# Optimization experiments

Hardware: AMD Instinct MI355X
Metric: run time of the kernel (lower is better)

## Reference

```python
import jax, jax.numpy as jnp
import numpy as np
from functools import partial

RED = 128      # reduced_dim
MK = 24        # r2d_m * r2d_k
HD, WD = 32, 16  # depth feature grid after 3 stride-2 convs on 256x128


def _conv(x, w, b):
    # torch Conv2d(k=3, stride=2, padding=1), NCHW / OIHW
    y = jax.lax.conv_general_dilated(
        x, w, window_strides=(2, 2), padding=((1, 1), (1, 1)),
        dimension_numbers=("NCHW", "OIHW", "NCHW"))
    return y + b[None, :, None, None]


def setup_inputs() -> dict:
    key = jax.random.key(0)
    ks = jax.random.split(key, 24)
    B = 64
    s = 0.02
    inp = {
        "features": jax.random.normal(ks[0], (B, 129, 768), jnp.float32),
        "d": jax.random.uniform(ks[1], (B, 1, 256, 128), jnp.float32),
        "W_rg": jax.random.normal(ks[2], (768, RED), jnp.float32) * s,
        "b_rg": jnp.zeros((RED,), jnp.float32),
        "W_rl": jax.random.normal(ks[3], (768, RED), jnp.float32) * s,
        "b_rl": jnp.zeros((RED,), jnp.float32),
        "conv1_w": jax.random.normal(ks[4], (64, 1, 3, 3), jnp.float32) * s,
        "conv1_b": jnp.zeros((64,), jnp.float32),
        "conv2_w": jax.random.normal(ks[5], (128, 64, 3, 3), jnp.float32) * s,
        "conv2_b": jnp.zeros((128,), jnp.float32),
        "conv3_w": jax.random.normal(ks[6], (128, 128, 3, 3), jnp.float32) * s,
        "conv3_b": jnp.zeros((128,), jnp.float32),
        "g_depth": jax.random.normal(ks[7], (RED,), jnp.float32),
        "W_merge": jax.random.normal(ks[8], (2 * RED, RED), jnp.float32) * s,
        "b_merge": jnp.zeros((RED,), jnp.float32),
        "W_q": jax.random.normal(ks[9], (2 * RED, RED), jnp.float32) * s,
        "b_q": jnp.zeros((RED,), jnp.float32),
        "W_v": jax.random.normal(ks[10], (RED, RED), jnp.float32) * s,
        "b_v": jnp.zeros((RED,), jnp.float32),
        "W_sel": jax.random.normal(ks[11], (RED, 3 * MK), jnp.float32) * s,
        "b_sel": jnp.zeros((3 * MK,), jnp.float32),
        "W_cls": jax.random.normal(ks[12], (RED, 751), jnp.float32) * s,
    }
    return inp


def _forward(features, d, W_rg, b_rg, W_rl, b_rl, conv1_w, conv1_b, conv2_w,
             conv2_b, conv3_w, conv3_b, g_depth, W_merge, b_merge, W_q, b_q,
             W_v, b_v, W_sel, b_sel, W_cls):
    B = features.shape[0]
    N = features.shape[1] - 1
    global_feat = features[:, 0] @ W_rg + b_rg                 # (B, 128)
    local_feat = features[:, 1:] @ W_rl + b_rl                 # (B, N, 128)
    lcg = jnp.concatenate(
        [jnp.broadcast_to(global_feat[:, None], (B, N, RED)), local_feat], -1)

    dep = _conv(_conv(_conv(d, conv1_w, conv1_b), conv2_w, conv2_b),
                conv3_w, conv3_b)                              # (B,128,32,16)
    dep = dep.transpose(0, 2, 3, 1).reshape(B, HD * WD, RED)
    lcgd = jnp.concatenate(
        [jnp.broadcast_to(g_depth[None, None], (B, HD * WD, RED)), dep], -1)
    lcgd = lcgd @ W_merge + b_merge

    q = lcg @ W_q + b_q                                        # (B,N,128)
    v = lcgd @ W_v + b_v                                       # (B,512,128)
    sel = jax.nn.sigmoid(q @ W_sel + b_sel)                    # (B,N,72)
    lx = sel[:, :, 0:2 * MK:2]                                 # (B,N,24)
    ly = sel[:, :, 1:2 * MK:2]
    attn = jax.nn.softmax(sel[:, :, 2 * MK:], axis=-1)

    # integer corner grid (original uses // stride == floor(loc*(dim-1)))
    x1 = jnp.floor(lx * (WD - 1))
    x2 = jnp.minimum(x1 + 1.0, float(WD - 1))
    y1 = jnp.floor(ly * (HD - 1))
    y2 = jnp.minimum(y1 + 1.0, float(HD - 1))
    xi1, xi2 = x1.astype(jnp.int32), x2.astype(jnp.int32)
    yi1, yi2 = y1.astype(jnp.int32), y2.astype(jnp.int32)

    # faithful to original gather: index = x_idx * Wd + y_idx
    gather = jax.vmap(lambda vb, ib: vb[ib])                   # (512,C),(N,K)->(N,K,C)
    f0 = gather(v, xi1 * WD + yi2)
    f1 = gather(v, xi2 * WD + yi2)
    f2 = gather(v, xi2 * WD + yi1)
    f3 = gather(v, xi1 * WD + yi1)

    # query coordinates scaled by full grid size (as in the original)
    x = lx * WD
    y = ly * HD
    w_ = x2 - x1
    h_ = y2 - y1
    degenerate = (h_ == 0) | (w_ == 0)
    denom = jnp.where(h_ * w_ == 0, 1.0, h_ * w_)
    coeff = jnp.where(degenerate, 2.0, 1.0 / denom)            # (B,N,24)
    xv0 = jnp.where(w_ == 0, 1.0, x2 - x)
    xv1 = jnp.where(w_ == 0, 1.0, x - x1)
    yv0 = jnp.where(h_ == 0, 1.0, y2 - y)
    yv1 = jnp.where(h_ == 0, 1.0, y - y1)

    # xv^T @ [[f0,f1],[f2,f3]] @ yv, per channel
    interp = coeff[..., None] * (
        xv0[..., None] * (f0 * yv0[..., None] + f1 * yv1[..., None]) +
        xv1[..., None] * (f2 * yv0[..., None] + f3 * yv1[..., None]))

    r2d_feat = jnp.mean(interp * attn[..., None], axis=-2)     # (B,N,128)
    final_embedding = jnp.mean(r2d_feat, axis=1)               # (B,128)
    cls_score = final_embedding @ W_cls                        # (B,751)
    return cls_score, final_embedding


def reference(features, d, W_rg, b_rg, W_rl, b_rl, conv1_w, conv1_b, conv2_w,
              conv2_b, conv3_w, conv3_b, g_depth, W_merge, b_merge, W_q, b_q,
              W_v, b_v, W_sel, b_sel, W_cls):
    return _forward(features, d, W_rg, b_rg, W_rl, b_rl, conv1_w, conv1_b,
                    conv2_w, conv2_b, conv3_w, conv3_b, g_depth, W_merge,
                    b_merge, W_q, b_q, W_v, b_v, W_sel, b_sel, W_cls)
```

## Files before the change

### kernel.cpp

```cpp
#include <hip/hip_runtime.h>
#include <hip/hip_bf16.h>


typedef __attribute__((ext_vector_type(8))) short short8;
typedef __attribute__((ext_vector_type(4))) short shortx4;
typedef __attribute__((ext_vector_type(4))) float floatx4;
typedef __attribute__((ext_vector_type(4))) int intx4;

#define MFMA16(a, b, c) __builtin_amdgcn_mfma_f32_16x16x32_bf16(a, b, c, 0, 0, 0)

__global__ __launch_bounds__(256) void prep_a(
    const float* __restrict__ W_q, const float* __restrict__ W_sel,
    const float* __restrict__ W_merge, const float* __restrict__ W_v,
    const float* __restrict__ g_depth, const float* __restrict__ b_merge,
    const float* __restrict__ features, const float* __restrict__ W_rg,
    const float* __restrict__ b_rg, const float* __restrict__ c2w,
    const float* __restrict__ c3w,
    float* __restrict__ W_qs, float* __restrict__ W_mv,
    float* __restrict__ c0, float* __restrict__ gfeat,
    __hip_bfloat16* __restrict__ w2t, __hip_bfloat16* __restrict__ w3t)
{
    __shared__ float fr_s[768];
    int bid = blockIdx.x, t = threadIdx.x;
    if (bid < 72) {
        int j = bid;
        float acc = 0.f;
        for (int k = 0; k < 128; ++k)
            acc = fmaf(W_q[t * 128 + k], W_sel[k * 72 + j], acc);
        W_qs[t * 72 + j] = acc;
    } else if (bid < 200) {
        int j = bid - 72;
        if (t < 128) {
            float acc = 0.f;
            for (int k = 0; k < 128; ++k)
                acc = fmaf(W_merge[(128 + t) * 128 + k], W_v[k * 128 + j], acc);
            W_mv[t * 128 + j] = acc;
        }
    } else if (bid == 200) {
        if (t < 128) {
            float acc = b_merge[t];
            for (int k = 0; k < 128; ++k)
                acc = fmaf(g_depth[k], W_merge[k * 128 + t], acc);
            c0[t] = acc;
        }
    } else if (bid < 265) {
        int row = bid - 201;
        for (int l = t; l < 768; l += 256)
            fr_s[l] = features[(long)row * 129 * 768 + l];
        __syncthreads();
        if (t < 128) {
            float acc = b_rg[t];
            for (int k = 0; k < 768; ++k)
                acc = fmaf(fr_s[k], W_rg[k * 128 + t], acc);
            gfeat[row * 128 + t] = acc;
        }
    } else if (bid < 553) {
        int idx = (bid - 265) * 256 + t;
        if (idx < 128 * 576) {
            int oc = idx / 576, k = idx % 576;
            int s = k >> 6, ic = k & 63;
            w2t[idx] = __float2bfloat16(c2w[oc * 576 + ic * 9 + s]);
        }
    } else {
        int idx = (bid - 553) * 256 + t;
        if (idx < 128 * 1152) {
            int oc = idx / 1152, k = idx % 1152;
            int s = k >> 7, ic = k & 127;
            w3t[idx] = __float2bfloat16(c3w[oc * 1152 + ic * 9 + s]);
        }
    }
}

__global__ __launch_bounds__(256) void prep2_k(
    const float* __restrict__ W_rl, const float* __restrict__ W_qs,
    const float* __restrict__ W_sel, const float* __restrict__ b_rl,
    const float* __restrict__ b_q, const float* __restrict__ b_sel,
    const float* __restrict__ gfeat, const float* __restrict__ c0,
    const float* __restrict__ W_v, const float* __restrict__ b_v,
    float* __restrict__ W_big, float* __restrict__ rowbias,
    float* __restrict__ c0v)
{
    int bid = blockIdx.x, t = threadIdx.x;
    if (bid < 216) {
        int j = bid / 3;
        int i = (bid % 3) * 256 + t;
        float acc = 0.f;
        for (int k = 0; k < 128; ++k)
            acc = fmaf(W_rl[i * 128 + k], W_qs[(128 + k) * 72 + j], acc);
        W_big[i * 72 + j] = acc;
    } else if (bid < 288) {
        int j = bid - 216;
        if (t < 64) {
            float vb = b_sel[j];
            for (int k = 0; k < 128; ++k) {
                vb = fmaf(b_rl[k], W_qs[(128 + k) * 72 + j], vb);
                vb = fmaf(b_q[k], W_sel[k * 72 + j], vb);
            }
            float acc = vb;
            for (int k = 0; k < 128; ++k)
                acc = fmaf(gfeat[t * 128 + k], W_qs[k * 72 + j], acc);
            rowbias[t * 72 + j] = acc;
        }
    } else {
        if (t < 128) {
            float acc = b_v[t];
            for (int k = 0; k < 128; ++k)
                acc = fmaf(c0[k], W_v[k * 128 + t], acc);
            c0v[t] = acc;
        }
    }
}

__global__ __launch_bounds__(256) void prep_b(
    const float* __restrict__ W_mv, const float* __restrict__ W_big,
    __hip_bfloat16* __restrict__ Bh, __hip_bfloat16* __restrict__ Bl,
    __hip_bfloat16* __restrict__ Wbh, __hip_bfloat16* __restrict__ Wbl)
{
    int bid = blockIdx.x, t = threadIdx.x;
    if (bid < 64) {
        int idx = bid * 256 + t;
        int n = idx >> 7, k = idx & 127;
        float w = W_mv[k * 128 + n];
        __hip_bfloat16 h = __float2bfloat16(w);
        Bh[idx] = h;
        Bl[idx] = __float2bfloat16(w - __bfloat162float(h));
    } else {
        int idx = (bid - 64) * 256 + t;
        if (idx < 80 * 768) {
            int n = idx / 768, k = idx - n * 768;
            float w = (n < 72) ? W_big[k * 72 + n] : 0.f;
            __hip_bfloat16 h = __float2bfloat16(w);
            Wbh[idx] = h;
            Wbl[idx] = __float2bfloat16(w - __bfloat162float(h));
        }
    }
}

__global__ __launch_bounds__(256) void conv1_k(
    const float* __restrict__ d, const float* __restrict__ w,
    const float* __restrict__ bias, __hip_bfloat16* __restrict__ out)
{
    __shared__ float in_s[9][130];
    __shared__ float ws_[576];
    __shared__ float bs_[64];
    int tid = threadIdx.x;
    int ohg = blockIdx.x & 31;
    int b   = blockIdx.x >> 5;
    int oh0 = ohg * 4;

    for (int l = tid; l < 576; l += 256) ws_[l] = w[l];
    if (tid < 64) bs_[tid] = bias[tid];
    for (int l = tid; l < 9 * 130; l += 256) {
        int r = l / 130, c = l - r * 130;
        int ih = 2 * oh0 - 1 + r;
        int iw = c - 1;
        float v = 0.f;
        if ((unsigned)ih < 256u && (unsigned)iw < 128u)
            v = d[(b * 256 + ih) * 128 + iw];
        in_s[r][c] = v;
    }
    __syncthreads();

    int ocg = tid & 7;
#pragma unroll
    for (int pb = 0; pb < 8; ++pb) {
        int pos = pb * 32 + (tid >> 3);
        int ohl = pos >> 6, ow = pos & 63;
        short8 res;
#pragma unroll
        for (int j = 0; j < 8; ++j) {
            int oc = ocg * 8 + j;
            float a = bs_[oc];
#pragma unroll
            for (int kh = 0; kh < 3; ++kh)
#pragma unroll
                for (int kw = 0; kw < 3; ++kw)
                    a = fmaf(in_s[2 * ohl + kh][2 * ow + kw],
                             ws_[oc * 9 + kh * 3 + kw], a);
            union { __hip_bfloat16 h; short s; } u;
            u.h = __float2bfloat16(a);
            res[j] = u.s;
        }
        long gpos = ((long)(b * 128 + oh0 + ohl) * 64 + ow);
        *(short8*)((short*)out + gpos * 64 + ocg * 8) = res;
    }
}

__global__ __launch_bounds__(256) void conv2_mfma(
    const __hip_bfloat16* __restrict__ in, const __hip_bfloat16* __restrict__ w2t,
    const float* __restrict__ bias, __hip_bfloat16* __restrict__ out)
{
    __shared__ short A_lds[128][72];
    __shared__ short B_lds[128][72];
    int tid = threadIdx.x;
    int oh0 = blockIdx.x * 4;
    int b   = blockIdx.y;
    int lane = tid & 63, wave = tid >> 6;
    int l16 = lane & 15, lh = lane >> 4;
    const short* inp = (const short*)in;
    const short* w2p = (const short*)w2t;

    floatx4 acc[2][8] = {};
    short8 av[4], bv[4];

#pragma unroll
    for (int i = 0; i < 4; ++i) {
        int c = tid + i * 256;
        int pos = c >> 3, seg = c & 7;
        int ohl = pos >> 5, ow = pos & 31;
        int ih = 2 * (oh0 + ohl) - 1;
        int iw = 2 * ow - 1;
        short8 v = {0,0,0,0,0,0,0,0};
        if ((unsigned)ih < 128u && (unsigned)iw < 64u)
            v = *(const short8*)(inp + (((long)(b * 128 + ih) * 64 + iw) * 64 + seg * 8));
        av[i] = v;
        bv[i] = *(const short8*)(w2p + pos * 576 + seg * 8);
    }

    for (int s = 0; s < 9; ++s) {
        __syncthreads();
#pragma unroll
        for (int i = 0; i < 4; ++i) {
            int c = tid + i * 256;
            int pos = c >> 3, seg = c & 7;
            *(short8*)&A_lds[pos][seg * 8] = av[i];
            *(short8*)&B_lds[pos][seg * 8] = bv[i];
        }
        __syncthreads();
        if (s < 8) {
            int sn = s + 1;
            int kh = sn / 3, kw = sn - kh * 3;
#pragma unroll
            for (int i = 0; i < 4; ++i) {
                int c = tid + i * 256;
                int pos = c >> 3, seg = c & 7;
                int ohl = pos >> 5, ow = pos & 31;
                int ih = 2 * (oh0 + ohl) - 1 + kh;
                int iw = 2 * ow - 1 + kw;
                short8 v = {0,0,0,0,0,0,0,0};
                if ((unsigned)ih < 128u && (unsigned)iw < 64u)
                    v = *(const short8*)(inp + (((long)(b * 128 + ih) * 64 + iw) * 64 + seg * 8));
                av[i] = v;
                bv[i] = *(const short8*)(w2p + pos * 576 + sn * 64 + seg * 8);
            }
        }
#pragma unroll
        for (int half = 0; half < 2; ++half) {
            short8 a0 = *(const short8*)&A_lds[wave * 32 + l16][half * 32 + lh * 8];
            short8 a1 = *(const short8*)&A_lds[wave * 32 + 16 + l16][half * 32 + lh * 8];
#pragma unroll
            for (int ni = 0; ni < 8; ++ni) {
                short8 bvf = *(const short8*)&B_lds[ni * 16 + l16][half * 32 + lh * 8];
                acc[0][ni] = MFMA16(a0, bvf, acc[0][ni]);
                acc[1][ni] = MFMA16(a1, bvf, acc[1][ni]);
            }
        }
    }

    float bf[8];
#pragma unroll
    for (int ni = 0; ni < 8; ++ni) bf[ni] = bias[ni * 16 + l16];
#pragma unroll
    for (int mi = 0; mi < 2; ++mi)
#pragma unroll
        for (int r = 0; r < 4; ++r) {
            int m = wave * 32 + mi * 16 + lh * 4 + r;
            int ohl = m >> 5, ow = m & 31;
            __hip_bfloat16* op = out + (((long)(b * 64 + oh0 + ohl) * 32) + ow) * 128;
#pragma unroll
            for (int ni = 0; ni < 8; ++ni) {
                int oc = ni * 16 + l16;
                op[oc] = __float2bfloat16(acc[mi][ni][r] + bf[ni]);
            }
        }
}

__global__ __launch_bounds__(256) void conv3_mfma(
    const __hip_bfloat16* __restrict__ in, const __hip_bfloat16* __restrict__ w3t,
    const float* __restrict__ bias, const __hip_bfloat16* __restrict__ Bh,
    const __hip_bfloat16* __restrict__ Bl, const float* __restrict__ c0v,
    float* __restrict__ v)
{
    __shared__ short A_lds[64][136];
    __shared__ short B_lds[128][136];
    int tid = threadIdx.x;
    int oh0 = blockIdx.x * 4;
    int b   = blockIdx.y;
    int lane = tid & 63, wave = tid >> 6;
    int wr = wave >> 1, wc = wave & 1;
    int l16 = lane & 15, lh = lane >> 4;
    const short* inp = (const short*)in;
    const short* w3p = (const short*)w3t;

    floatx4 acc[2][4] = {};
    short8 av[4], bv[8];

#pragma unroll
    for (int i = 0; i < 4; ++i) {
        int c = tid + i * 256;
        int pos = c >> 4, seg = c & 15;
        int oa = pos >> 4, ow = pos & 15;
        int ih = 2 * (oh0 + oa) - 1;
        int iw = 2 * ow - 1;
        short8 vv = {0,0,0,0,0,0,0,0};
        if ((unsigned)ih < 64u && (unsigned)iw < 32u)
            vv = *(const short8*)(inp + (((long)(b * 64 + ih) * 32 + iw) * 128 + seg * 8));
        av[i] = vv;
    }
#pragma unroll
    for (int i = 0; i < 8; ++i) {
        int c = tid + i * 256;
        int oc = c >> 4, seg = c & 15;
        bv[i] = *(const short8*)(w3p + oc * 1152 + seg * 8);
    }

    for (int s = 0; s < 9; ++s) {
        __syncthreads();
#pragma unroll
        for (int i = 0; i < 4; ++i) {
            int c = tid + i * 256;
            int pos = c >> 4, seg = c & 15;
            *(short8*)&A_lds[pos][seg * 8] = av[i];
        }
#pragma unroll
        for (int i = 0; i < 8; ++i) {
            int c = tid + i * 256;
            int oc = c >> 4, seg = c & 15;
            *(short8*)&B_lds[oc][seg * 8] = bv[i];
        }
        __syncthreads();
        if (s < 8) {
            int sn = s + 1;
            int kh = sn / 3, kw = sn - kh * 3;
#pragma unroll
            for (int i = 0; i < 4; ++i) {
                int c = tid + i * 256;
                int pos = c >> 4, seg = c & 15;
                int oa = pos >> 4, ow = pos & 15;
                int ih = 2 * (oh0 + oa) - 1 + kh;
                int iw = 2 * ow - 1 + kw;
                short8 vv = {0,0,0,0,0,0,0,0};
                if ((unsigned)ih < 64u && (unsigned)iw < 32u)
                    vv = *(const short8*)(inp + (((long)(b * 64 + ih) * 32 + iw) * 128 + seg * 8));
                av[i] = vv;
            }
#pragma unroll
            for (int i = 0; i < 8; ++i) {
                int c = tid + i * 256;
                int oc = c >> 4, seg = c & 15;
                bv[i] = *(const short8*)(w3p + oc * 1152 + sn * 128 + seg * 8);
            }
        }
#pragma unroll
        for (int ks = 0; ks < 4; ++ks) {
            short8 a0 = *(const short8*)&A_lds[wr * 32 + l16][ks * 32 + lh * 8];
            short8 a1 = *(const short8*)&A_lds[wr * 32 + 16 + l16][ks * 32 + lh * 8];
#pragma unroll
            for (int ni = 0; ni < 4; ++ni) {
                short8 bvf = *(const short8*)&B_lds[wc * 64 + ni * 16 + l16][ks * 32 + lh * 8];
                acc[0][ni] = MFMA16(a0, bvf, acc[0][ni]);
                acc[1][ni] = MFMA16(a1, bvf, acc[1][ni]);
            }
        }
    }

    float bf[4];
#pragma unroll
    for (int ni = 0; ni < 4; ++ni) bf[ni] = bias[wc * 64 + ni * 16 + l16];

    __syncthreads();
    short (*Dh)[136] = A_lds;
    short (*Dl)[136] = B_lds;
#pragma unroll
    for (int mi = 0; mi < 2; ++mi)
#pragma unroll
        for (int r = 0; r < 4; ++r) {
            int m = wr * 32 + mi * 16 + lh * 4 + r;
#pragma unroll
            for (int ni = 0; ni < 4; ++ni) {
                int oc = wc * 64 + ni * 16 + l16;
                float f = acc[mi][ni][r] + bf[ni];
                union { __hip_bfloat16 bb; short ss; } uh, ul;
                uh.bb = __float2bfloat16(f);
                ul.bb = __float2bfloat16(f - __bfloat162float(uh.bb));
                Dh[m][oc] = uh.ss;
                Dl[m][oc] = ul.ss;
            }
        }
    __syncthreads();

    floatx4 vacc[2][4] = {};
#pragma unroll
    for (int kk = 0; kk < 4; ++kk) {
        short8 ah[2], al[2];
#pragma unroll
        for (int mi = 0; mi < 2; ++mi) {
            ah[mi] = *(const short8*)&Dh[wr * 32 + mi * 16 + l16][kk * 32 + lh * 8];
            al[mi] = *(const short8*)&Dl[wr * 32 + mi * 16 + l16][kk * 32 + lh * 8];
        }
#pragma unroll
        for (int nf = 0; nf < 4; ++nf) {
            int gn = wc * 64 + nf * 16 + l16;
            short8 bh = *(const short8*)((const short*)Bh + gn * 128 + kk * 32 + lh * 8);
            short8 bl = *(const short8*)((const short*)Bl + gn * 128 + kk * 32 + lh * 8);
#pragma unroll
            for (int mi = 0; mi < 2; ++mi) {
                vacc[mi][nf] = MFMA16(ah[mi], bh, vacc[mi][nf]);
                vacc[mi][nf] = MFMA16(al[mi], bh, vacc[mi][nf]);
                vacc[mi][nf] = MFMA16(ah[mi], bl, vacc[mi][nf]);
            }
        }
    }
#pragma unroll
    for (int nf = 0; nf < 4; ++nf) {
        int gn = wc * 64 + nf * 16 + l16;
        float cv = c0v[gn];
#pragma unroll
        for (int mi = 0; mi < 2; ++mi)
#pragma unroll
            for (int r = 0; r < 4; ++r) {
                int m = wr * 32 + mi * 16 + lh * 4 + r;
                v[((long)(b * 512 + oh0 * 16 + m)) * 128 + gn] = vacc[mi][nf][r] + cv;
            }
    }
}

__global__ __launch_bounds__(256) void selbw_k(
    const float* __restrict__ F, const __hip_bfloat16* __restrict__ Wbh,
    const __hip_bfloat16* __restrict__ Wbl, const float* __restrict__ rowbias,
    int* __restrict__ idxb, float* __restrict__ wtb)
{
    __shared__ short Ah[16][136];
    __shared__ short Al[16][136];
    __shared__ float slx[16][24], sly[16][24], satt[16][24];
    int tid = threadIdx.x;
    int m0 = blockIdx.x * 16;
    int padd = (m0 >> 7) + 1;
    int lane = tid & 63, wave = tid >> 6;
    int l16 = lane & 15, lh = lane >> 4;

    int sr = tid >> 4, sc = (tid & 15) * 8;
    const float* fsrc = F + (long)(m0 + sr + padd) * 768 + sc;

    floatx4 acc0 = {0.f, 0.f, 0.f, 0.f};
    floatx4 acc1 = {0.f, 0.f, 0.f, 0.f};
    bool two = (wave == 3);
    const short* bhp = (const short*)Wbh;
    const short* blp = (const short*)Wbl;
    int gn0 = wave * 16 + l16;
    int gn1 = 64 + l16;

    float4 f0 = *(const float4*)(fsrc);
    float4 f1 = *(const float4*)(fsrc + 4);

    for (int c = 0; c < 6; ++c) {
        shortx4 h0, l0, h1, l1;
#pragma unroll
        for (int i = 0; i < 4; ++i) {
            union { __hip_bfloat16 b; short s; } uh, ul;
            float fa = (&f0.x)[i];
            uh.b = __float2bfloat16(fa);
            ul.b = __float2bfloat16(fa - __bfloat162float(uh.b));
            h0[i] = uh.s; l0[i] = ul.s;
            float fb = (&f1.x)[i];
            uh.b = __float2bfloat16(fb);
            ul.b = __float2bfloat16(fb - __bfloat162float(uh.b));
            h1[i] = uh.s; l1[i] = ul.s;
        }
        __syncthreads();
        *(shortx4*)&Ah[sr][sc]     = h0;
        *(shortx4*)&Ah[sr][sc + 4] = h1;
        *(shortx4*)&Al[sr][sc]     = l0;
        *(shortx4*)&Al[sr][sc + 4] = l1;
        __syncthreads();
        if (c < 5) {
            f0 = *(const float4*)(fsrc + (c + 1) * 128);
            f1 = *(const float4*)(fsrc + (c + 1) * 128 + 4);
        }
#pragma unroll
        for (int ks = 0; ks < 4; ++ks) {
            short8 ah = *(const short8*)&Ah[l16][ks * 32 + lh * 8];
            short8 al = *(const short8*)&Al[l16][ks * 32 + lh * 8];
            int koff = c * 128 + ks * 32 + lh * 8;
            short8 bh0 = *(const short8*)(bhp + gn0 * 768 + koff);
            short8 bl0 = *(const short8*)(blp + gn0 * 768 + koff);
            acc0 = MFMA16(ah, bh0, acc0);
            acc0 = MFMA16(al, bh0, acc0);
            acc0 = MFMA16(ah, bl0, acc0);
            if (two) {
                short8 bh1 = *(const short8*)(bhp + gn1 * 768 + koff);
                short8 bl1 = *(const short8*)(blp + gn1 * 768 + koff);
                acc1 = MFMA16(ah, bh1, acc1);
                acc1 = MFMA16(al, bh1, acc1);
                acc1 = MFMA16(ah, bl1, acc1);
            }
        }
    }

    if (wave < 3) {
        int j = wave * 16 + l16;
#pragma unroll
        for (int r = 0; r < 4; ++r) {
            int rl = lh * 4 + r;
            float val = acc0[r] + rowbias[((m0 + rl) >> 7) * 72 + j];
            float sg = 1.f / (1.f + expf(-val));
            if (j & 1) sly[rl][j >> 1] = sg;
            else       slx[rl][j >> 1] = sg;
        }
    } else {
#pragma unroll
        for (int r = 0; r < 4; ++r) {
            int rl = lh * 4 + r;
            int b72 = ((m0 + rl) >> 7) * 72;
            float s0 = 1.f / (1.f + expf(-(acc0[r] + rowbias[b72 + 48 + l16])));
            float s1 = -1e30f;
            if (l16 < 8)
                s1 = 1.f / (1.f + expf(-(acc1[r] + rowbias[b72 + 64 + l16])));
            float mx = fmaxf(s0, s1);
#pragma unroll
            for (int s = 1; s < 16; s <<= 1)
                mx = fmaxf(mx, __shfl_xor(mx, s));
            float e0 = expf(s0 - mx);
            float e1 = (l16 < 8) ? expf(s1 - mx) : 0.f;
            float sum = e0 + e1;
#pragma unroll
            for (int s = 1; s < 16; s <<= 1)
                sum += __shfl_xor(sum, s);
            satt[rl][l16] = e0 / sum;
            if (l16 < 8) satt[rl][16 + l16] = e1 / sum;
        }
    }
    __syncthreads();

    for (int e = tid; e < 384; e += 256) {
        int rl = e / 24, k = e - rl * 24;
        int row = m0 + rl;
        float lxv = slx[rl][k], lyv = sly[rl][k];
        float a = satt[rl][k] * (1.f / 24.f);
        float x1 = floorf(lxv * 15.f), x2 = fminf(x1 + 1.f, 15.f);
        float y1 = floorf(lyv * 31.f), y2 = fminf(y1 + 1.f, 31.f);
        int xi1 = (int)x1, xi2 = (int)x2, yi1 = (int)y1, yi2 = (int)y2;
        float x = lxv * 16.f, y = lyv * 32.f;
        float w_ = x2 - x1, h_ = y2 - y1;
        float hwp = h_ * w_;
        bool deg = (h_ == 0.f) || (w_ == 0.f);
        float denom = (hwp == 0.f) ? 1.f : hwp;
        float coeff = (deg ? 2.f : 1.f / denom) * a;
        float xv0 = (w_ == 0.f) ? 1.f : (x2 - x);
        float xv1 = (w_ == 0.f) ? 1.f : (x - x1);
        float yv0 = (h_ == 0.f) ? 1.f : (y2 - y);
        float yv1 = (h_ == 0.f) ? 1.f : (y - y1);
        intx4 iv; floatx4 wv;
        iv[0] = (xi1 * 16 + yi2) * 128;
        iv[1] = (xi2 * 16 + yi2) * 128;
        iv[2] = (xi2 * 16 + yi1) * 128;
        iv[3] = (xi1 * 16 + yi1) * 128;
        wv[0] = coeff * xv0 * yv0;
        wv[1] = coeff * xv0 * yv1;
        wv[2] = coeff * xv1 * yv0;
        wv[3] = coeff * xv1 * yv1;
        *(intx4*)&idxb[(long)row * 96 + k * 4] = iv;
        *(floatx4*)&wtb[(long)row * 96 + k * 4] = wv;
    }
}

__global__ __launch_bounds__(256) void r2d_k(
    const float* __restrict__ v, const int* __restrict__ idxb,
    const float* __restrict__ wtb, float* __restrict__ r2d)
{
    int rg = blockIdx.x;
    int b  = blockIdx.y;
    int tid = threadIdx.x;
    int c  = tid & 127;
    int rp = tid >> 7;
    __shared__ int sidx[8][96];
    __shared__ float swt[8][96];
    for (int l = tid; l < 8 * 96; l += 256) {
        int rr = l / 96, e = l - rr * 96;
        long base = ((long)(b * 128 + rg * 8 + rr)) * 96 + e;
        sidx[rr][e] = idxb[base];
        swt[rr][e]  = wtb[base];
    }
    __syncthreads();
    const float* vb = v + (long)b * 512 * 128 + c;
#pragma unroll
    for (int it = 0; it < 4; ++it) {
        int rr = it * 2 + rp;
        const int* si = sidx[rr];
        const float* sw = swt[rr];
        float acc = 0.f;
#pragma unroll
        for (int k = 0; k < 24; ++k) {
            float v0 = vb[si[k * 4 + 0]];
            float v1 = vb[si[k * 4 + 1]];
            float v2 = vb[si[k * 4 + 2]];
            float v3 = vb[si[k * 4 + 3]];
            acc = fmaf(sw[k * 4 + 0], v0, acc);
            acc = fmaf(sw[k * 4 + 1], v1, acc);
            acc = fmaf(sw[k * 4 + 2], v2, acc);
            acc = fmaf(sw[k * 4 + 3], v3, acc);
        }
        r2d[((long)(b * 128 + rg * 8 + rr)) * 128 + c] = acc;
    }
}

__global__ __launch_bounds__(256) void fecls_k(
    const float* __restrict__ r2d, const float* __restrict__ W_cls,
    float* __restrict__ out)
{
    __shared__ float fe_s[128];
    int b = blockIdx.x, t = threadIdx.x;
    if (t < 128) {
        float acc = 0.f;
        for (int nn = 0; nn < 128; ++nn)
            acc += r2d[((long)b * 128 + nn) * 128 + t];
        acc *= (1.f / 128.f);
        fe_s[t] = acc;
        out[64 * 751 + b * 128 + t] = acc;
    }
    __syncthreads();
    for (int j = t; j < 751; j += 256) {
        float acc = 0.f;
        for (int k = 0; k < 128; ++k)
            acc = fmaf(fe_s[k], W_cls[k * 751 + j], acc);
        out[b * 751 + j] = acc;
    }
}

extern "C" void kernel_launch(void* const* d_in, const int* in_sizes, int n_in,
                              void* d_out, int out_size, void* d_ws, size_t ws_size,
                              hipStream_t stream)
{
    const float* features = (const float*)d_in[0];
    const float* d        = (const float*)d_in[1];
    const float* W_rg  = (const float*)d_in[2];
    const float* b_rg  = (const float*)d_in[3];
    const float* W_rl  = (const float*)d_in[4];
    const float* b_rl  = (const float*)d_in[5];
    const float* c1w   = (const float*)d_in[6];
    const float* c1b   = (const float*)d_in[7];
    const float* c2w   = (const float*)d_in[8];
    const float* c2b   = (const float*)d_in[9];
    const float* c3w   = (const float*)d_in[10];
    const float* c3b   = (const float*)d_in[11];
    const float* g_depth = (const float*)d_in[12];
    const float* W_merge = (const float*)d_in[13];
    const float* b_merge = (const float*)d_in[14];
    const float* W_q   = (const float*)d_in[15];
    const float* b_q   = (const float*)d_in[16];
    const float* W_v   = (const float*)d_in[17];
    const float* b_v   = (const float*)d_in[18];
    const float* W_sel = (const float*)d_in[19];
    const float* b_sel = (const float*)d_in[20];
    const float* W_cls = (const float*)d_in[21];
    float* out = (float*)d_out;

    char* ws = (char*)d_ws;
    __hip_bfloat16* c1 = (__hip_bfloat16*)(ws + 0);
    float* v      = (float*)(ws + 33554432);
    __hip_bfloat16* c2 = (__hip_bfloat16*)(ws + 67108864);
    __hip_bfloat16* w2t = (__hip_bfloat16*)(ws + 100663296);
    __hip_bfloat16* w3t = (__hip_bfloat16*)(ws + 100810752);
    float* W_qs    = (float*)(ws + 101105664);
    float* W_mv    = (float*)(ws + 101179392);
    float* W_big   = (float*)(ws + 101244928);
    float* rowbias = (float*)(ws + 101466112);
    float* c0b     = (float*)(ws + 101484544);
    float* c0v     = (float*)(ws + 101485056);
    float* gfeat   = (float*)(ws + 101485568);
    __hip_bfloat16* Wmv_bh = (__hip_bfloat16*)(ws + 101518336);
    __hip_bfloat16* Wmv_bl = (__hip_bfloat16*)(ws + 101551104);
    __hip_bfloat16* Wbig_h = (__hip_bfloat16*)(ws + 101583872);
    __hip_bfloat16* Wbig_l = (__hip_bfloat16*)(ws + 101706752);
    int*   idxb   = (int*)(ws + 101832704);
    float* wtb    = (float*)(ws + 104978432);
    float* r2d    = (float*)(ws + 113836544);

    prep_a<<<1129, 256, 0, stream>>>(W_q, W_sel, W_merge, W_v, g_depth, b_merge,
                                     features, W_rg, b_rg, c2w, c3w,
                                     W_qs, W_mv, c0b, gfeat, w2t, w3t);
    prep2_k<<<289, 256, 0, stream>>>(W_rl, W_qs, W_sel, b_rl, b_q, b_sel,
                                     gfeat, c0b, W_v, b_v, W_big, rowbias, c0v);
    prep_b<<<304, 256, 0, stream>>>(W_mv, W_big, Wmv_bh, Wmv_bl, Wbig_h, Wbig_l);

    conv1_k<<<2048, 256, 0, stream>>>(d, c1w, c1b, c1);
    conv2_mfma<<<dim3(16, 64), 256, 0, stream>>>(c1, w2t, c2b, c2);
    conv3_mfma<<<dim3(8, 64), 256, 0, stream>>>(c2, w3t, c3b,
                                                Wmv_bh, Wmv_bl, c0v, v);

    selbw_k<<<512, 256, 0, stream>>>(features, Wbig_h, Wbig_l, rowbias,
                                     idxb, wtb);

    r2d_k<<<dim3(16, 64), 256, 0, stream>>>(v, idxb, wtb, r2d);
    fecls_k<<<64, 256, 0, stream>>>(r2d, W_cls, out);
}
```

Measured before the change: 204.4 us.

## Stage per-batch value slice in LDS for bilinear gather in r2d kernel

The r2d gather kernel now assigns each block a 16-channel slice of one batch's value map, stages all 512 positions of that slice in shared memory (padded to stride 20), and loops over eight chunks of 16 rows. It gathers from LDS instead of issuing scattered global loads. Index entries are rescaled to point into the LDS tile. The grid shrinks to 8x64 blocks, each using about 53KB of LDS, so occupancy drops and idx/wt tables are re-read by each of the 8 channel-slice blocks.

Measured after the change: 220.8 us. 1.08x slower.

```diff
diff --git a/kernel.cpp b/kernel.cpp
--- a/kernel.cpp
+++ b/kernel.cpp
@@ -568,39 +568,46 @@
     const float* __restrict__ v, const int* __restrict__ idxb,
     const float* __restrict__ wtb, float* __restrict__ r2d)
 {
-    int rg = blockIdx.x;
+    __shared__ float vs[512][20];
+    __shared__ int  sidx[16][96];
+    __shared__ float swt[16][96];
+    int cq = blockIdx.x;
     int b  = blockIdx.y;
     int tid = threadIdx.x;
-    int c  = tid & 127;
-    int rp = tid >> 7;
-    __shared__ int sidx[8][96];
-    __shared__ float swt[8][96];
-    for (int l = tid; l < 8 * 96; l += 256) {
-        int rr = l / 96, e = l - rr * 96;
-        long base = ((long)(b * 128 + rg * 8 + rr)) * 96 + e;
-        sidx[rr][e] = idxb[base];
-        swt[rr][e]  = wtb[base];
-    }
-    __syncthreads();
-    const float* vb = v + (long)b * 512 * 128 + c;
-#pragma unroll
-    for (int it = 0; it < 4; ++it) {
-        int rr = it * 2 + rp;
+
+    const float* vbase = v + (long)b * 65536 + cq * 16;
+    for (int f = tid; f < 2048; f += 256) {
+        int pos = f >> 2, fc = (f & 3) * 4;
+        float4 t4 = *(const float4*)(vbase + (long)pos * 128 + fc);
+        *(float4*)&vs[pos][fc] = t4;
+    }
+
+    int cc = tid & 15, rr = tid >> 4;
+    const float* vf = &vs[0][0];
+    for (int ch = 0; ch < 8; ++ch) {
+        __syncthreads();
+        for (int l = tid; l < 16 * 96; l += 256) {
+            int r = l / 96, e = l - r * 96;
+            long base = ((long)(b * 128 + ch * 16 + r)) * 96 + e;
+            sidx[r][e] = (idxb[base] >> 7) * 20;
+            swt[r][e]  = wtb[base];
+        }
+        __syncthreads();
         const int* si = sidx[rr];
         const float* sw = swt[rr];
         float acc = 0.f;
 #pragma unroll
         for (int k = 0; k < 24; ++k) {
-            float v0 = vb[si[k * 4 + 0]];
-            float v1 = vb[si[k * 4 + 1]];
-            float v2 = vb[si[k * 4 + 2]];
-            float v3 = vb[si[k * 4 + 3]];
+            float v0 = vf[si[k * 4 + 0] + cc];
+            float v1 = vf[si[k * 4 + 1] + cc];
+            float v2 = vf[si[k * 4 + 2] + cc];
+            float v3 = vf[si[k * 4 + 3] + cc];
             acc = fmaf(sw[k * 4 + 0], v0, acc);
             acc = fmaf(sw[k * 4 + 1], v1, acc);
             acc = fmaf(sw[k * 4 + 2], v2, acc);
             acc = fmaf(sw[k * 4 + 3], v3, acc);
         }
-        r2d[((long)(b * 128 + rg * 8 + rr)) * 128 + c] = acc;
+        r2d[((long)(b * 128 + ch * 16 + rr)) * 128 + cq * 16 + cc] = acc;
     }
 }
 
@@ -691,6 +698,6 @@
     selbw_k<<<512, 256, 0, stream>>>(features, Wbig_h, Wbig_l, rowbias,
                                      idxb, wtb);
 
-    r2d_k<<<dim3(16, 64), 256, 0, stream>>>(v, idxb, wtb, r2d);
+    r2d_k<<<dim3(8, 64), 256, 0, stream>>>(v, idxb, wtb, r2d);
     fecls_k<<<64, 256, 0, stream>>>(r2d, W_cls, out);
 }
```
